# Kernel tuning notes

Measured on AMD Instinct MI355X. Metric: run time of the kernel, lower is better.

## Reference

```python
import jax, jax.numpy as jnp
import numpy as np

N = 50000   # nodes
E = 800000  # edges
F_IN, F_HID, F_OUT = 128, 96, 40


def setup_inputs() -> dict:
    key = jax.random.key(0)
    ks = jax.random.split(key, 9)
    x = jax.random.normal(ks[0], (N, F_IN), dtype=jnp.float32)
    edge_index = jax.random.randint(ks[1], (2, E), 0, N, dtype=jnp.int32)
    def lin(k, fi, fo):
        s = 1.0 / np.sqrt(fi)
        return jax.random.uniform(k, (fi, fo), jnp.float32, -s, s)
    W1 = lin(ks[2], F_IN, F_HID)
    b1 = jnp.zeros((F_HID,), jnp.float32)
    W2 = lin(ks[3], F_HID, F_HID)
    b2 = jnp.zeros((F_HID,), jnp.float32)
    Wout = lin(ks[4], F_HID, F_OUT)
    bout = jnp.zeros((F_OUT,), jnp.float32)
    return {"x": x, "edge_index": edge_index, "W1": W1, "b1": b1,
            "W2": W2, "b2": b2, "Wout": Wout, "bout": bout}


def _gcn_norm(edge_index, n):
    # add self-loops, symmetric degree normalization (PyG GCNConv default)
    loops = jnp.arange(n, dtype=edge_index.dtype)
    src = jnp.concatenate([edge_index[0], loops])
    dst = jnp.concatenate([edge_index[1], loops])
    deg = jax.ops.segment_sum(jnp.ones_like(dst, dtype=jnp.float32), dst,
                              num_segments=n)
    dinv = jnp.where(deg > 0, jax.lax.rsqrt(deg), 0.0)
    norm = dinv[src] * dinv[dst]   # [E+N]
    return src, dst, norm


def _gcn_layer(h, src, dst, norm, W, b, n):
    # linear transform, then normalized scatter-add aggregation, then bias
    h = h @ W                                 # [N, Fout]
    msg = h[src] * norm[:, None]              # gather + scale
    agg = jax.ops.segment_sum(msg, dst, num_segments=n)
    return agg + b


def reference(x, edge_index, W1, b1, W2, b2, Wout, bout):
    n = x.shape[0]
    src, dst, norm = _gcn_norm(edge_index, n)
    h = jax.nn.relu(_gcn_layer(x, src, dst, norm, W1, b1, n))
    h = jax.nn.relu(_gcn_layer(h, src, dst, norm, W2, b2, n))
    return h @ Wout + bout
```

## Files before the change

kernel.cpp:

```cpp
#include <hip/hip_runtime.h>
#include <hip/hip_fp16.h>

#define N_NODES 50000
#define N_EDGES 800000
#define F_INN   128
#define F_HID   96
#define F_OUTT  40

typedef _Float16 half8 __attribute__((ext_vector_type(8)));
typedef float    floatx4 __attribute__((ext_vector_type(4)));

template <int FI, typename TIN>
__device__ __forceinline__ void mfma_gemm_body(
        const TIN* __restrict__ X, const __half* __restrict__ BTg,
        float4* __restrict__ Th4, int n, int bx) {
    __shared__ __half BTl[96 * 136];
    __half* OUTl = BTl;
    int tid = threadIdx.x;
    {
        const int4* s = reinterpret_cast<const int4*>(BTg);
        int4* d = reinterpret_cast<int4*>(BTl);
        for (int i = tid; i < 96 * 136 / 8; i += 256) d[i] = s[i];
    }
    __syncthreads();

    int lane = tid & 63, w = tid >> 6;
    int lm = lane & 15, q = lane >> 4;
    int base = bx * 64 + w * 16;
    int node = base + lm;
    int nclamp = min(node, n - 1);
    const TIN* Xrow = X + (size_t)nclamp * FI;

    floatx4 cf[6];
    #pragma unroll
    for (int t = 0; t < 6; ++t) cf[t] = (floatx4){0.f, 0.f, 0.f, 0.f};

    constexpr int KS = FI / 32;
    #pragma unroll
    for (int ks = 0; ks < KS; ++ks) {
        half8 bv;
        if constexpr (sizeof(TIN) == 4) {
            const float4* xr = reinterpret_cast<const float4*>(Xrow + 32 * ks + q * 8);
            float4 f0 = xr[0], f1 = xr[1];
            union { half8 v; __half2 h[4]; } b;
            b.h[0] = __floats2half2_rn(f0.x, f0.y);
            b.h[1] = __floats2half2_rn(f0.z, f0.w);
            b.h[2] = __floats2half2_rn(f1.x, f1.y);
            b.h[3] = __floats2half2_rn(f1.z, f1.w);
            bv = b.v;
        } else {
            bv = *reinterpret_cast<const half8*>(Xrow + 32 * ks + q * 8);
        }
        #pragma unroll
        for (int t = 0; t < 6; ++t) {
            half8 a = *reinterpret_cast<const half8*>(
                &BTl[(t * 16 + lm) * 136 + q * 8 + 32 * ks]);
            cf[t] = __builtin_amdgcn_mfma_f32_16x16x32_f16(a, bv, cf[t], 0, 0, 0);
        }
    }

    __syncthreads();

    __half* orow = OUTl + (w * 16 + lm) * 104;
    #pragma unroll
    for (int t = 0; t < 6; ++t) {
        union { int2 i2; __half2 h[2]; } u;
        u.h[0] = __floats2half2_rn(cf[t][0], cf[t][1]);
        u.h[1] = __floats2half2_rn(cf[t][2], cf[t][3]);
        *reinterpret_cast<int2*>(&orow[t * 16 + q * 4]) = u.i2;
    }
    #pragma unroll
    for (int R = 0; R < 3; ++R) {
        int nl = lane >> 2, c = (lane & 3) + 4 * R;
        float4 v = *reinterpret_cast<const float4*>(&OUTl[(w * 16 + nl) * 104 + c * 8]);
        int gn = base + nl;
        if (gn < n) Th4[(size_t)gn * 12 + c] = v;
    }
}

__global__ __launch_bounds__(256) void count_gemm1_kernel(
        const int* __restrict__ dst, int* __restrict__ counts8, int* __restrict__ rank,
        int e, const float* __restrict__ X, const __half* __restrict__ BT1,
        float4* __restrict__ Th4, int n, int nCB) {
    if ((int)blockIdx.x < nCB) {
        int sh = blockIdx.x & 7;
        int* cnt = counts8 + sh * N_NODES;
        int i = blockIdx.x * 512 + threadIdx.x;
        int j = i + 256;
        int di = 0, dj = 0, ri, rj;
        bool bi = i < e, bj = j < e;
        if (bi) di = dst[i];
        if (bj) dj = dst[j];
        if (bi) ri = atomicAdd(&cnt[di], 1);
        if (bj) rj = atomicAdd(&cnt[dj], 1);
        if (bi) rank[i] = ri;
        if (bj) rank[j] = rj;
    } else {
        mfma_gemm_body<F_INN, float>(X, BT1, Th4, n, blockIdx.x - nCB);
    }
}

template <int FI, typename TIN>
__global__ __launch_bounds__(256) void mfma_gemm_kernel(
        const TIN* __restrict__ X, const __half* __restrict__ BTg,
        float4* __restrict__ Th4, int n) {
    mfma_gemm_body<FI, TIN>(X, BTg, Th4, n, blockIdx.x);
}

__global__ void wt_kernel(const float* __restrict__ W1, const float* __restrict__ W2,
                          __half* __restrict__ BT1, __half* __restrict__ BT2) {
    int i = blockIdx.x * 256 + threadIdx.x;
    if (i < 96 * 128) {
        int j = i / 128, k = i - j * 128;
        BT1[j * 136 + k] = __float2half(W1[k * 96 + j]);
    } else if (i < 96 * 128 + 96 * 96) {
        int t = i - 96 * 128;
        int j = t / 96, k = t - j * 96;
        BT2[j * 136 + k] = __float2half(W2[k * 96 + j]);
    }
}

__global__ __launch_bounds__(1024) void scan_local_kernel(
        const int* __restrict__ counts8, int* __restrict__ row_start,
        float* __restrict__ dinv, int* __restrict__ blk_sums, int n) {
    __shared__ int wave_sums[16];
    int tid = threadIdx.x, lane = tid & 63, wid = tid >> 6;
    int i = blockIdx.x * 1024 + tid;
    int v = 0;
    if (i < n) {
        #pragma unroll
        for (int s = 0; s < 8; ++s) v += counts8[s * N_NODES + i];
    }
    int val = v;
    #pragma unroll
    for (int off = 1; off < 64; off <<= 1) {
        int u = __shfl_up(val, off, 64);
        if (lane >= off) val += u;
    }
    if (lane == 63) wave_sums[wid] = val;
    __syncthreads();
    if (wid == 0) {
        int w = (lane < 16) ? wave_sums[lane] : 0;
        #pragma unroll
        for (int off = 1; off < 16; off <<= 1) {
            int u = __shfl_up(w, off, 64);
            if (lane >= off) w += u;
        }
        if (lane < 16) wave_sums[lane] = w;
    }
    __syncthreads();
    int excl = ((wid == 0) ? 0 : wave_sums[wid - 1]) + (val - v);
    if (i < n) {
        row_start[i] = excl;
        dinv[i] = rsqrtf((float)(v + 1));
    }
    if (tid == 0) blk_sums[blockIdx.x] = wave_sums[15];
}

__global__ __launch_bounds__(1024) void scan_apply_kernel(
        int* __restrict__ row_start, const int* __restrict__ blk_sums,
        const int* __restrict__ counts8, int* __restrict__ base8, int n, int nblk) {
    __shared__ int s_my, s_tot;
    int tid = threadIdx.x;
    if (tid < 64) {
        int v = (tid < nblk) ? blk_sums[tid] : 0;
        int val = v;
        #pragma unroll
        for (int off = 1; off < 64; off <<= 1) {
            int u = __shfl_up(val, off, 64);
            if (tid >= off) val += u;
        }
        if (tid == (int)blockIdx.x) s_my = val - v;
        if (tid == 63) s_tot = val;
    }
    __syncthreads();
    int i = blockIdx.x * 1024 + tid;
    if (i < n) {
        int b = row_start[i] + s_my;
        row_start[i] = b;
        int run = b;
        #pragma unroll
        for (int s = 0; s < 8; ++s) {
            base8[s * N_NODES + i] = run;
            run += counts8[s * N_NODES + i];
        }
    }
    if (blockIdx.x == 0 && tid == 0) row_start[n] = s_tot;
}

__global__ void fill_csr_kernel(const int* __restrict__ src, const int* __restrict__ dst,
                                const int* __restrict__ rank, const int* __restrict__ base8,
                                int* __restrict__ csr_src, int e) {
    int i = blockIdx.x * blockDim.x + threadIdx.x;
    if (i >= e) return;
    int sh = (i >> 9) & 7;
    csr_src[base8[sh * N_NODES + dst[i]] + rank[i]] = src[i];
}

__global__ __launch_bounds__(256) void agg_kernel(
        const __half2* __restrict__ T, const int* __restrict__ row_start,
        const int* __restrict__ csr_src, const float* __restrict__ dinv,
        const float* __restrict__ bias, __half2* __restrict__ H, int n) {
    int lane = threadIdx.x & 63;
    int node = __builtin_amdgcn_readfirstlane(blockIdx.x * 4 + (threadIdx.x >> 6));
    if (node >= n) return;
    int fl = min(lane, 47);

    float dn = dinv[node];
    float2 self = __half22float2(T[(size_t)node * 48 + fl]);
    float accx = dn * self.x, accy = dn * self.y;

    int idx = row_start[node];
    int end = row_start[node + 1];
    for (; idx + 8 <= end; idx += 8) {
        int s[8];
        #pragma unroll
        for (int u = 0; u < 8; ++u) s[u] = csr_src[idx + u];
        float ws[8];
        #pragma unroll
        for (int u = 0; u < 8; ++u) ws[u] = dinv[s[u]];
        float2 f[8];
        #pragma unroll
        for (int u = 0; u < 8; ++u) f[u] = __half22float2(T[(size_t)s[u] * 48 + fl]);
        #pragma unroll
        for (int u = 0; u < 8; ++u) {
            accx = fmaf(ws[u], f[u].x, accx);
            accy = fmaf(ws[u], f[u].y, accy);
        }
    }
    for (; idx < end; ++idx) {
        int s = csr_src[idx];
        float w = dinv[s];
        float2 f = __half22float2(T[(size_t)s * 48 + fl]);
        accx = fmaf(w, f.x, accx);
        accy = fmaf(w, f.y, accy);
    }
    if (lane < 48) {
        float2 b = reinterpret_cast<const float2*>(bias)[lane];
        float ox = fmaxf(fmaf(dn, accx, b.x), 0.f);
        float oy = fmaxf(fmaf(dn, accy, b.y), 0.f);
        H[(size_t)node * 48 + lane] = __floats2half2_rn(ox, oy);
    }
}

__global__ __launch_bounds__(320) void gemm_out_kernel(
        const __half2* __restrict__ A, const float* __restrict__ W,
        const float* __restrict__ bias, float* __restrict__ C, int n) {
    __shared__ float Wlds[96 * 40];
    int tid = threadIdx.y * 10 + threadIdx.x;
    for (int i = tid; i < 96 * 10; i += 320)
        reinterpret_cast<float4*>(Wlds)[i] = reinterpret_cast<const float4*>(W)[i];
    __syncthreads();

    int j    = threadIdx.x * 4;
    int node = blockIdx.x * 32 + threadIdx.y;
    int nc   = min(node, n - 1);
    const __half2* Ah = A + (size_t)nc * 48;
    float4 acc = make_float4(0.f, 0.f, 0.f, 0.f);
    for (int k2 = 0; k2 < 48; k2 += 2) {
        float2 a01 = __half22float2(Ah[k2]);
        float2 a23 = __half22float2(Ah[k2 + 1]);
        int k = 2 * k2;
        float4 w0 = *reinterpret_cast<const float4*>(Wlds + (k + 0) * 40 + j);
        float4 w1 = *reinterpret_cast<const float4*>(Wlds + (k + 1) * 40 + j);
        float4 w2 = *reinterpret_cast<const float4*>(Wlds + (k + 2) * 40 + j);
        float4 w3 = *reinterpret_cast<const float4*>(Wlds + (k + 3) * 40 + j);
        acc.x += a01.x * w0.x + a01.y * w1.x + a23.x * w2.x + a23.y * w3.x;
        acc.y += a01.x * w0.y + a01.y * w1.y + a23.x * w2.y + a23.y * w3.y;
        acc.z += a01.x * w0.z + a01.y * w1.z + a23.x * w2.z + a23.y * w3.z;
        acc.w += a01.x * w0.w + a01.y * w1.w + a23.x * w2.w + a23.y * w3.w;
    }
    if (node < n) {
        float4 b = *reinterpret_cast<const float4*>(bias + j);
        acc.x += b.x; acc.y += b.y; acc.z += b.z; acc.w += b.w;
        *reinterpret_cast<float4*>(C + (size_t)node * 40 + j) = acc;
    }
}


extern "C" void kernel_launch(void* const* d_in, const int* in_sizes, int n_in,
                              void* d_out, int out_size, void* d_ws, size_t ws_size,
                              hipStream_t stream) {
    const float* x    = (const float*)d_in[0];
    const int*   ei   = (const int*)d_in[1];
    const float* W1   = (const float*)d_in[2];
    const float* b1   = (const float*)d_in[3];
    const float* W2   = (const float*)d_in[4];
    const float* b2   = (const float*)d_in[5];
    const float* Wout = (const float*)d_in[6];
    const float* bout = (const float*)d_in[7];
    float*       out  = (float*)d_out;

    const int* src = ei;
    const int* dst = ei + N_EDGES;

    char* ws = (char*)d_ws;
    size_t off = 0;
    auto alloc = [&](size_t bytes) {
        size_t o = off;
        off = (off + bytes + 511) & ~(size_t)511;
        return (void*)(ws + o);
    };
    int*     counts8   = (int*)    alloc((size_t)8 * N_NODES * sizeof(int));
    int*     base8     = (int*)    alloc((size_t)8 * N_NODES * sizeof(int));
    int*     row_start = (int*)    alloc((N_NODES + 1) * sizeof(int));
    float*   dinv      = (float*)  alloc(N_NODES * sizeof(float));
    int*     blk_sums  = (int*)    alloc(64 * sizeof(int));
    int*     rank      = (int*)    alloc((size_t)N_EDGES * sizeof(int));
    int*     csr_src   = (int*)    alloc((size_t)N_EDGES * sizeof(int));
    __half*  BT1       = (__half*) alloc((size_t)96 * 136 * sizeof(__half));
    __half*  BT2       = (__half*) alloc((size_t)96 * 136 * sizeof(__half));
    __half2* Th        = (__half2*)alloc((size_t)N_NODES * 48 * sizeof(__half2));
    __half2* Hh        = (__half2*)alloc((size_t)N_NODES * 48 * sizeof(__half2));

    const int NSCAN = (N_NODES + 1023) / 1024;
    const int CB2   = (N_EDGES + 511) / 512;
    const int FB    = (N_EDGES + 255) / 256;
    const int GB    = (N_NODES + 63) / 64;

    hipMemsetAsync(counts8, 0, (size_t)8 * N_NODES * sizeof(int), stream);
    wt_kernel<<<(96 * 128 + 96 * 96 + 255) / 256, 256, 0, stream>>>(W1, W2, BT1, BT2);

    count_gemm1_kernel<<<CB2 + GB, 256, 0, stream>>>(
        dst, counts8, rank, N_EDGES, x, BT1, (float4*)Th, N_NODES, CB2);

    scan_local_kernel<<<NSCAN, 1024, 0, stream>>>(
        counts8, row_start, dinv, blk_sums, N_NODES);
    scan_apply_kernel<<<NSCAN, 1024, 0, stream>>>(
        row_start, blk_sums, counts8, base8, N_NODES, NSCAN);
    fill_csr_kernel<<<FB, 256, 0, stream>>>(
        src, dst, rank, base8, csr_src, N_EDGES);

    agg_kernel<<<(N_NODES + 3) / 4, 256, 0, stream>>>(
        Th, row_start, csr_src, dinv, b1, Hh, N_NODES);

    mfma_gemm_kernel<F_HID, __half><<<GB, 256, 0, stream>>>(
        (const __half*)Hh, BT2, (float4*)Th, N_NODES);
    agg_kernel<<<(N_NODES + 3) / 4, 256, 0, stream>>>(
        Th, row_start, csr_src, dinv, b2, Hh, N_NODES);

    gemm_out_kernel<<<(N_NODES + 31) / 32, dim3(10, 32), 0, stream>>>(
        Hh, Wout, bout, out, N_NODES);
}
```

Measured before the change: 228.6 us.

## Prescale transformed features by source dinv to drop per-edge dinv gathers

Moves the source-side degree normalization out of the aggregation loop. The layer-1 features are scaled by dinv in a scale pass fused into the CSR fill kernel, and the layer-2 features are scaled in the GEMM epilogue. The aggregation kernels then do plain sums, with no per-edge dinv[src] gather or multiply. The cost is an extra read-modify-write pass over the layer-1 features, and rounding to fp16 now happens after scaling.

```diff
diff --git a/kernel.cpp b/kernel.cpp
--- a/kernel.cpp
+++ b/kernel.cpp
@@ -10,10 +10,10 @@
 typedef _Float16 half8 __attribute__((ext_vector_type(8)));
 typedef float    floatx4 __attribute__((ext_vector_type(4)));
 
-template <int FI, typename TIN>
+template <int FI, typename TIN, bool SCALE>
 __device__ __forceinline__ void mfma_gemm_body(
         const TIN* __restrict__ X, const __half* __restrict__ BTg,
-        float4* __restrict__ Th4, int n, int bx) {
+        const float* __restrict__ dinv, float4* __restrict__ Th4, int n, int bx) {
     __shared__ __half BTl[96 * 136];
     __half* OUTl = BTl;
     int tid = threadIdx.x;
@@ -59,14 +59,17 @@
         }
     }
 
+    float dv = 1.0f;
+    if constexpr (SCALE) dv = dinv[nclamp];
+
     __syncthreads();
 
     __half* orow = OUTl + (w * 16 + lm) * 104;
     #pragma unroll
     for (int t = 0; t < 6; ++t) {
         union { int2 i2; __half2 h[2]; } u;
-        u.h[0] = __floats2half2_rn(cf[t][0], cf[t][1]);
-        u.h[1] = __floats2half2_rn(cf[t][2], cf[t][3]);
+        u.h[0] = __floats2half2_rn(dv * cf[t][0], dv * cf[t][1]);
+        u.h[1] = __floats2half2_rn(dv * cf[t][2], dv * cf[t][3]);
         *reinterpret_cast<int2*>(&orow[t * 16 + q * 4]) = u.i2;
     }
     #pragma unroll
@@ -96,15 +99,15 @@
         if (bi) rank[i] = ri;
         if (bj) rank[j] = rj;
     } else {
-        mfma_gemm_body<F_INN, float>(X, BT1, Th4, n, blockIdx.x - nCB);
-    }
-}
-
-template <int FI, typename TIN>
+        mfma_gemm_body<F_INN, float, false>(X, BT1, nullptr, Th4, n, blockIdx.x - nCB);
+    }
+}
+
+template <int FI, typename TIN, bool SCALE>
 __global__ __launch_bounds__(256) void mfma_gemm_kernel(
         const TIN* __restrict__ X, const __half* __restrict__ BTg,
-        float4* __restrict__ Th4, int n) {
-    mfma_gemm_body<FI, TIN>(X, BTg, Th4, n, blockIdx.x);
+        const float* __restrict__ dinv, float4* __restrict__ Th4, int n) {
+    mfma_gemm_body<FI, TIN, SCALE>(X, BTg, dinv, Th4, n, blockIdx.x);
 }
 
 __global__ void wt_kernel(const float* __restrict__ W1, const float* __restrict__ W2,
@@ -188,13 +191,30 @@
     if (blockIdx.x == 0 && tid == 0) row_start[n] = s_tot;
 }
 
-__global__ void fill_csr_kernel(const int* __restrict__ src, const int* __restrict__ dst,
-                                const int* __restrict__ rank, const int* __restrict__ base8,
-                                int* __restrict__ csr_src, int e) {
-    int i = blockIdx.x * blockDim.x + threadIdx.x;
-    if (i >= e) return;
-    int sh = (i >> 9) & 7;
-    csr_src[base8[sh * N_NODES + dst[i]] + rank[i]] = src[i];
+__global__ __launch_bounds__(256) void fill_scale_kernel(
+        const int* __restrict__ src, const int* __restrict__ dst,
+        const int* __restrict__ rank, const int* __restrict__ base8,
+        int* __restrict__ csr_src, const float* __restrict__ dinv,
+        float4* __restrict__ Th4, int e, int nFB) {
+    if ((int)blockIdx.x < nFB) {
+        int i = blockIdx.x * 256 + threadIdx.x;
+        if (i >= e) return;
+        int sh = (i >> 9) & 7;
+        csr_src[base8[sh * N_NODES + dst[i]] + rank[i]] = src[i];
+    } else {
+        int i = (blockIdx.x - nFB) * 256 + threadIdx.x;
+        if (i >= N_NODES * 12) return;
+        int node = i / 12;
+        float s = dinv[node];
+        union { float4 f4; __half2 h[4]; } u;
+        u.f4 = Th4[i];
+        #pragma unroll
+        for (int q = 0; q < 4; ++q) {
+            float2 t = __half22float2(u.h[q]);
+            u.h[q] = __floats2half2_rn(s * t.x, s * t.y);
+        }
+        Th4[i] = u.f4;
+    }
 }
 
 __global__ __launch_bounds__(256) void agg_kernel(
@@ -208,7 +228,7 @@
 
     float dn = dinv[node];
     float2 self = __half22float2(T[(size_t)node * 48 + fl]);
-    float accx = dn * self.x, accy = dn * self.y;
+    float accx = self.x, accy = self.y;
 
     int idx = row_start[node];
     int end = row_start[node + 1];
@@ -216,24 +236,20 @@
         int s[8];
         #pragma unroll
         for (int u = 0; u < 8; ++u) s[u] = csr_src[idx + u];
-        float ws[8];
-        #pragma unroll
-        for (int u = 0; u < 8; ++u) ws[u] = dinv[s[u]];
         float2 f[8];
         #pragma unroll
         for (int u = 0; u < 8; ++u) f[u] = __half22float2(T[(size_t)s[u] * 48 + fl]);
         #pragma unroll
         for (int u = 0; u < 8; ++u) {
-            accx = fmaf(ws[u], f[u].x, accx);
-            accy = fmaf(ws[u], f[u].y, accy);
+            accx += f[u].x;
+            accy += f[u].y;
         }
     }
     for (; idx < end; ++idx) {
         int s = csr_src[idx];
-        float w = dinv[s];
         float2 f = __half22float2(T[(size_t)s * 48 + fl]);
-        accx = fmaf(w, f.x, accx);
-        accy = fmaf(w, f.y, accy);
+        accx += f.x;
+        accy += f.y;
     }
     if (lane < 48) {
         float2 b = reinterpret_cast<const float2*>(bias)[lane];
@@ -316,6 +332,7 @@
     const int NSCAN = (N_NODES + 1023) / 1024;
     const int CB2   = (N_EDGES + 511) / 512;
     const int FB    = (N_EDGES + 255) / 256;
+    const int SB    = (N_NODES * 12 + 255) / 256;
     const int GB    = (N_NODES + 63) / 64;
 
     hipMemsetAsync(counts8, 0, (size_t)8 * N_NODES * sizeof(int), stream);
@@ -328,14 +345,14 @@
         counts8, row_start, dinv, blk_sums, N_NODES);
     scan_apply_kernel<<<NSCAN, 1024, 0, stream>>>(
         row_start, blk_sums, counts8, base8, N_NODES, NSCAN);
-    fill_csr_kernel<<<FB, 256, 0, stream>>>(
-        src, dst, rank, base8, csr_src, N_EDGES);
+    fill_scale_kernel<<<FB + SB, 256, 0, stream>>>(
+        src, dst, rank, base8, csr_src, dinv, (float4*)Th, N_EDGES, FB);
 
     agg_kernel<<<(N_NODES + 3) / 4, 256, 0, stream>>>(
         Th, row_start, csr_src, dinv, b1, Hh, N_NODES);
 
-    mfma_gemm_kernel<F_HID, __half><<<GB, 256, 0, stream>>>(
-        (const __half*)Hh, BT2, (float4*)Th, N_NODES);
+    mfma_gemm_kernel<F_HID, __half, true><<<GB, 256, 0, stream>>>(
+        (const __half*)Hh, BT2, dinv, (float4*)Th, N_NODES);
     agg_kernel<<<(N_NODES + 3) / 4, 256, 0, stream>>>(
         Th, row_start, csr_src, dinv, b2, Hh, N_NODES);
 
```

Result: no change. 226.2 us (-1.0%).
